# Kernel tuning notes

Measured on AMD Instinct MI355X. Metric: run time of the kernel, lower is better.

The kernel has to match this reference:

```python
import jax, jax.numpy as jnp
import numpy as np

N_NODES = 100000
N_EDGES = 3200000
EMB_DIM = 128


def setup_inputs() -> dict:
    key = jax.random.key(0)
    k_emb, k_w1, k_w2, k_e = jax.random.split(key, 4)
    emb = jax.random.normal(k_emb, (N_NODES, EMB_DIM), dtype=jnp.float32)
    W1 = jax.random.normal(k_w1, (EMB_DIM, 64), dtype=jnp.float32) * (1.0 / np.sqrt(EMB_DIM))
    b1 = jnp.zeros((64,), dtype=jnp.float32)
    W2 = jax.random.normal(k_w2, (64, 32), dtype=jnp.float32) * (1.0 / np.sqrt(64))
    b2 = jnp.zeros((32,), dtype=jnp.float32)
    edge_index = jax.random.randint(k_e, (2, N_EDGES), 0, N_NODES, dtype=jnp.int64)
    return {"embedding": emb, "W1": W1, "b1": b1, "W2": W2, "b2": b2,
            "edge_index": edge_index}


def gcn_conv(x, W, b, src, dst, n):
    # PyG GCNConv defaults: add self-loops, symmetric normalization D^-1/2 (A+I) D^-1/2,
    # linear transform first, then gather-scale-scatter aggregation, then bias.
    xw = x @ W                                                  # [N, out]
    ones = jnp.ones(src.shape, dtype=xw.dtype)
    deg = jax.ops.segment_sum(ones, dst, num_segments=n) + 1.0  # in-degree + self-loop
    dis = jax.lax.rsqrt(deg)                                    # deg >= 1 always
    norm = dis[src] * dis[dst]                                  # [E]
    agg = jax.ops.segment_sum(xw[src] * norm[:, None], dst, num_segments=n)
    agg = agg + (dis * dis)[:, None] * xw                       # self-loop messages
    return agg + b


def reference(embedding, W1, b1, W2, b2, edge_index):
    n = embedding.shape[0]
    src, dst = edge_index[0], edge_index[1]
    # encode
    h = jax.nn.relu(gcn_conv(embedding, W1, b1, src, dst, n))
    z = gcn_conv(h, W2, b2, src, dst, n)                        # [N, 32]
    # decode: per-edge gather-dot-sigmoid
    logits = jnp.sum(z[src] * z[dst], axis=1)                   # [E]
    return jax.nn.sigmoid(logits)
```

## Files before the change

### kernel.cpp

```cpp
#include <hip/hip_runtime.h>
#include <hip/hip_bf16.h>
#include <math.h>

#define NN 100000
#define NE 3200000
#define NPAD 100096
#define NB 196
#define BN 512
#define EPB 8192
#define NBLK 391

typedef __attribute__((ext_vector_type(8))) short short8;
typedef __attribute__((ext_vector_type(4))) float floatx4;
typedef __attribute__((ext_vector_type(4))) unsigned uint4v;

__device__ __forceinline__ unsigned short bf16_of(float x) {
    __hip_bfloat16 h = __float2bfloat16(x);
    return *(unsigned short*)&h;
}
__device__ __forceinline__ unsigned pack2(float a, float b) {
    return (unsigned)bf16_of(a) | ((unsigned)bf16_of(b) << 16);
}
__device__ __forceinline__ float lo_f(unsigned u) { return __uint_as_float(u << 16); }
__device__ __forceinline__ float hi_f(unsigned u) { return __uint_as_float(u & 0xffff0000u); }
__device__ __forceinline__ void acc8(float* a, uint4v r) {
    a[0] += lo_f(r[0]); a[1] += hi_f(r[0]);
    a[2] += lo_f(r[1]); a[3] += hi_f(r[1]);
    a[4] += lo_f(r[2]); a[5] += hi_f(r[2]);
    a[6] += lo_f(r[3]); a[7] += hi_f(r[3]);
}

__global__ __launch_bounds__(256) void hist_kernel(const int* __restrict__ dst,
                                                   int* __restrict__ blkhist) {
    __shared__ int cnt[NB];
    int t = threadIdx.x;
    for (int i = t; i < NB; i += 256) cnt[i] = 0;
    __syncthreads();
    int e0 = blockIdx.x * EPB;
    int e1 = min(e0 + EPB, NE);
    for (int e = e0 + t; e < e1; e += 256) atomicAdd(&cnt[dst[e] >> 9], 1);
    __syncthreads();
    for (int i = t; i < NB; i += 256) blkhist[i * NBLK + blockIdx.x] = cnt[i];
}

__global__ __launch_bounds__(64) void scanA_kernel(int* __restrict__ blkhist,
                                                   int* __restrict__ totals) {
    int j = blockIdx.x, lane = threadIdx.x;
    int base = j * NBLK;
    int carry = 0;
    for (int c = 0; c < NBLK; c += 64) {
        int b = c + lane;
        int v = (b < NBLK) ? blkhist[base + b] : 0;
        int inc = v;
#pragma unroll
        for (int m = 1; m < 64; m <<= 1) {
            int u = __shfl_up(inc, m, 64);
            if (lane >= m) inc += u;
        }
        if (b < NBLK) blkhist[base + b] = carry + inc - v;
        carry += __shfl(inc, 63, 64);
    }
    if (lane == 0) totals[j] = carry;
}

__global__ __launch_bounds__(256) void scanB_kernel(const int* __restrict__ totals,
                                                    int* __restrict__ bucket_base) {
    __shared__ int sm[NB];
    int t = threadIdx.x;
    if (t < NB) sm[t] = totals[t];
    __syncthreads();
    if (t == 0) {
        int r = 0;
        for (int i = 0; i < NB; ++i) { bucket_base[i] = r; r += sm[i]; }
        bucket_base[NB] = r;
    }
}

__global__ __launch_bounds__(256) void scatter_kernel(const int* __restrict__ src,
                                                      const int* __restrict__ dst,
                                                      const int* __restrict__ blkhist,
                                                      const int* __restrict__ bucket_base,
                                                      int* __restrict__ staged) {
    __shared__ int cnt[NB];
    __shared__ int lbase[NB + 1];
    __shared__ int gbase[NB];
    __shared__ int sbuf[EPB];
    __shared__ unsigned char sbkt[EPB];
    int t = threadIdx.x;
    for (int i = t; i < NB; i += 256) cnt[i] = 0;
    __syncthreads();
    int e0 = blockIdx.x * EPB;
    int e1 = min(e0 + EPB, NE);
    int cn = e1 - e0;
    for (int e = e0 + t; e < e1; e += 256) atomicAdd(&cnt[dst[e] >> 9], 1);
    __syncthreads();
    if (t < 64) {
        int v[4]; int s = 0;
#pragma unroll
        for (int k = 0; k < 4; ++k) { int idx = t * 4 + k; v[k] = (idx < NB) ? cnt[idx] : 0; s += v[k]; }
        int inc = s;
#pragma unroll
        for (int m = 1; m < 64; m <<= 1) {
            int u = __shfl_up(inc, m, 64);
            if (t >= m) inc += u;
        }
        int run = inc - s;
#pragma unroll
        for (int k = 0; k < 4; ++k) { int idx = t * 4 + k; if (idx < NB) lbase[idx] = run; run += v[k]; }
        if (t == 63) lbase[NB] = inc;
    }
    __syncthreads();
    for (int i = t; i < NB; i += 256) {
        gbase[i] = bucket_base[i] + blkhist[i * NBLK + blockIdx.x];
        cnt[i] = lbase[i];
    }
    __syncthreads();
    for (int e = e0 + t; e < e1; e += 256) {
        int s = src[e], d = dst[e];
        int bk = d >> 9;
        int r = atomicAdd(&cnt[bk], 1);
        sbuf[r] = (s << 9) | (d & (BN - 1));
        sbkt[r] = (unsigned char)bk;
    }
    __syncthreads();
    for (int i = t; i < cn; i += 256) {
        int bk = sbkt[i];
        staged[gbase[bk] + i - lbase[bk]] = sbuf[i];
    }
}

__global__ __launch_bounds__(256) void fine_kernel(const int* __restrict__ staged,
                                                   const int* __restrict__ bucket_base,
                                                   int* __restrict__ offset,
                                                   float* __restrict__ dis,
                                                   int* __restrict__ csr_src) {
    __shared__ int hist[BN];
    __shared__ int offs[BN];
    __shared__ int cur[BN];
    int t = threadIdx.x, j = blockIdx.x;
    int bb = bucket_base[j], be = bucket_base[j + 1];
    for (int i = t; i < BN; i += 256) hist[i] = 0;
    __syncthreads();
    for (int e = bb + t; e < be; e += 256) atomicAdd(&hist[staged[e] & (BN - 1)], 1);
    __syncthreads();
    if (t < 64) {
        int v[8]; int s = 0;
#pragma unroll
        for (int k = 0; k < 8; ++k) { v[k] = hist[t * 8 + k]; s += v[k]; }
        int inc = s;
#pragma unroll
        for (int m = 1; m < 64; m <<= 1) {
            int u = __shfl_up(inc, m, 64);
            if (t >= m) inc += u;
        }
        int run = inc - s;
#pragma unroll
        for (int k = 0; k < 8; ++k) { offs[t * 8 + k] = run; run += v[k]; }
    }
    __syncthreads();
    for (int l = t; l < BN; l += 256) {
        cur[l] = offs[l];
        int n = j * BN + l;
        if (n < NN) {
            offset[n] = bb + offs[l];
            dis[n] = rsqrtf((float)hist[l] + 1.0f);
        }
    }
    if (j == NB - 1 && t == 0) offset[NN] = NE;
    __syncthreads();
    for (int e = bb + t; e < be; e += 256) {
        int p = staged[e];
        int r = atomicAdd(&cur[p & (BN - 1)], 1);
        csr_src[bb + r] = p >> 9;
    }
}

__global__ __launch_bounds__(256) void mm1_kernel(const float* __restrict__ x,
                                                  const float* __restrict__ W,
                                                  const float* __restrict__ dis,
                                                  unsigned short* __restrict__ y) {
    __shared__ unsigned short Wt[64][136];
    int t = threadIdx.x;
    for (int i = t; i < 128 * 64; i += 256) {
        int k = i >> 6, n = i & 63;
        Wt[n][k] = bf16_of(W[i]);
    }
    __syncthreads();
    int wave = t >> 6, lane = t & 63;
    int quad = lane >> 4, n16 = lane & 15;
    short8 bfr[4][4];
#pragma unroll
    for (int s = 0; s < 4; ++s)
#pragma unroll
        for (int tt = 0; tt < 4; ++tt)
            bfr[s][tt] = *(const short8*)&Wt[tt * 16 + n16][s * 32 + quad * 8];
    int tile0 = (blockIdx.x * 4 + wave) * 4;
#pragma unroll 1
    for (int it = 0; it < 4; ++it) {
        int tile = tile0 + it;
        if (tile >= 6250) break;
        int m0 = tile * 16;
        const float* xp = x + (size_t)(m0 + n16) * 128 + quad * 8;
        floatx4 acc0 = {0,0,0,0}, acc1 = {0,0,0,0}, acc2 = {0,0,0,0}, acc3 = {0,0,0,0};
#pragma unroll
        for (int s = 0; s < 4; ++s) {
            floatx4 lo = __builtin_nontemporal_load((const floatx4*)(xp + s * 32));
            floatx4 hi = __builtin_nontemporal_load((const floatx4*)(xp + s * 32 + 4));
            short8 a;
            a[0] = (short)bf16_of(lo[0]); a[1] = (short)bf16_of(lo[1]);
            a[2] = (short)bf16_of(lo[2]); a[3] = (short)bf16_of(lo[3]);
            a[4] = (short)bf16_of(hi[0]); a[5] = (short)bf16_of(hi[1]);
            a[6] = (short)bf16_of(hi[2]); a[7] = (short)bf16_of(hi[3]);
            acc0 = __builtin_amdgcn_mfma_f32_16x16x32_bf16(a, bfr[s][0], acc0, 0, 0, 0);
            acc1 = __builtin_amdgcn_mfma_f32_16x16x32_bf16(a, bfr[s][1], acc1, 0, 0, 0);
            acc2 = __builtin_amdgcn_mfma_f32_16x16x32_bf16(a, bfr[s][2], acc2, 0, 0, 0);
            acc3 = __builtin_amdgcn_mfma_f32_16x16x32_bf16(a, bfr[s][3], acc3, 0, 0, 0);
        }
#pragma unroll
        for (int r = 0; r < 4; ++r) {
            int ro = m0 + quad * 4 + r;
            float sc = dis[ro];
            unsigned short* yp = y + (size_t)ro * 64 + n16;
            yp[0]  = bf16_of(acc0[r] * sc);
            yp[16] = bf16_of(acc1[r] * sc);
            yp[32] = bf16_of(acc2[r] * sc);
            yp[48] = bf16_of(acc3[r] * sc);
        }
    }
}

__global__ __launch_bounds__(256) void mm2_kernel(const unsigned short* __restrict__ h,
                                                  const float* __restrict__ W,
                                                  const float* __restrict__ dis,
                                                  unsigned short* __restrict__ y) {
    __shared__ unsigned short Wt[32][72];
    int t = threadIdx.x;
    for (int i = t; i < 64 * 32; i += 256) {
        int k = i >> 5, n = i & 31;
        Wt[n][k] = bf16_of(W[i]);
    }
    __syncthreads();
    int wave = t >> 6, lane = t & 63;
    int quad = lane >> 4, n16 = lane & 15;
    short8 bfr[2][2];
#pragma unroll
    for (int s = 0; s < 2; ++s)
#pragma unroll
        for (int tt = 0; tt < 2; ++tt)
            bfr[s][tt] = *(const short8*)&Wt[tt * 16 + n16][s * 32 + quad * 8];
    int tile0 = (blockIdx.x * 4 + wave) * 4;
#pragma unroll 1
    for (int it = 0; it < 4; ++it) {
        int tile = tile0 + it;
        if (tile >= 6250) break;
        int m0 = tile * 16;
        const unsigned short* hp = h + (size_t)(m0 + n16) * 64 + quad * 8;
        floatx4 acc0 = {0,0,0,0}, acc1 = {0,0,0,0};
#pragma unroll
        for (int s = 0; s < 2; ++s) {
            short8 a = *(const short8*)(hp + s * 32);
            acc0 = __builtin_amdgcn_mfma_f32_16x16x32_bf16(a, bfr[s][0], acc0, 0, 0, 0);
            acc1 = __builtin_amdgcn_mfma_f32_16x16x32_bf16(a, bfr[s][1], acc1, 0, 0, 0);
        }
#pragma unroll
        for (int r = 0; r < 4; ++r) {
            int ro = m0 + quad * 4 + r;
            float sc = dis[ro];
            unsigned short* yp = y + (size_t)ro * 32 + n16;
            yp[0]  = bf16_of(acc0[r] * sc);
            yp[16] = bf16_of(acc1[r] * sc);
        }
    }
}

__global__ __launch_bounds__(256) void agg64_kernel(const uint4v* __restrict__ ys4,
                                                    const float* __restrict__ dis,
                                                    const int* __restrict__ offset,
                                                    const int* __restrict__ csr_src,
                                                    const float* __restrict__ b,
                                                    uint4v* __restrict__ h4) {
    int tid = blockIdx.x * 256 + threadIdx.x;
    int nd = tid >> 3, c = tid & 7;
    if (nd >= NN) return;
    int start = offset[nd], end = offset[nd + 1];
    float acc[8] = {0, 0, 0, 0, 0, 0, 0, 0};
    acc8(acc, ys4[(size_t)nd * 8 + c]);
    if (start < end) {
        int last = end - 1;
        int sk[8];
#pragma unroll
        for (int k = 0; k < 8; ++k) sk[k] = csr_src[min(start + k, last)];
        for (int i = start; i < end; i += 8) {
            uint4v r0 = ys4[(size_t)sk[0] * 8 + c];
            uint4v r1 = ys4[(size_t)sk[1] * 8 + c];
            uint4v r2 = ys4[(size_t)sk[2] * 8 + c];
            uint4v r3 = ys4[(size_t)sk[3] * 8 + c];
            uint4v r4 = ys4[(size_t)sk[4] * 8 + c];
            uint4v r5 = ys4[(size_t)sk[5] * 8 + c];
            uint4v r6 = ys4[(size_t)sk[6] * 8 + c];
            uint4v r7 = ys4[(size_t)sk[7] * 8 + c];
            int i2 = i + 8;
            if (i2 < end) {
#pragma unroll
                for (int k = 0; k < 8; ++k) sk[k] = csr_src[min(i2 + k, last)];
            }
            int rem = end - i;
            acc8(acc, r0);
            if (rem > 1) acc8(acc, r1);
            if (rem > 2) acc8(acc, r2);
            if (rem > 3) acc8(acc, r3);
            if (rem > 4) acc8(acc, r4);
            if (rem > 5) acc8(acc, r5);
            if (rem > 6) acc8(acc, r6);
            if (rem > 7) acc8(acc, r7);
        }
    }
    float ds = dis[nd];
    const float4 bv0 = *(const float4*)&b[c * 8];
    const float4 bv1 = *(const float4*)&b[c * 8 + 4];
    uint4v o;
    o[0] = pack2(fmaxf(fmaf(ds, acc[0], bv0.x), 0.f), fmaxf(fmaf(ds, acc[1], bv0.y), 0.f));
    o[1] = pack2(fmaxf(fmaf(ds, acc[2], bv0.z), 0.f), fmaxf(fmaf(ds, acc[3], bv0.w), 0.f));
    o[2] = pack2(fmaxf(fmaf(ds, acc[4], bv1.x), 0.f), fmaxf(fmaf(ds, acc[5], bv1.y), 0.f));
    o[3] = pack2(fmaxf(fmaf(ds, acc[6], bv1.z), 0.f), fmaxf(fmaf(ds, acc[7], bv1.w), 0.f));
    __builtin_nontemporal_store(o, &h4[(size_t)nd * 8 + c]);
}

__global__ __launch_bounds__(256) void agg32_kernel(const uint4v* __restrict__ ys4,
                                                    const float* __restrict__ dis,
                                                    const int* __restrict__ offset,
                                                    const int* __restrict__ csr_src,
                                                    const float* __restrict__ b,
                                                    uint4v* __restrict__ z4) {
    int tid = blockIdx.x * 256 + threadIdx.x;
    int nd = tid >> 2, c = tid & 3;
    if (nd >= NN) return;
    int start = offset[nd], end = offset[nd + 1];
    float acc[8] = {0, 0, 0, 0, 0, 0, 0, 0};
    acc8(acc, ys4[(size_t)nd * 4 + c]);
    if (start < end) {
        int last = end - 1;
        int sk[8];
#pragma unroll
        for (int k = 0; k < 8; ++k) sk[k] = csr_src[min(start + k, last)];
        for (int i = start; i < end; i += 8) {
            uint4v r0 = ys4[(size_t)sk[0] * 4 + c];
            uint4v r1 = ys4[(size_t)sk[1] * 4 + c];
            uint4v r2 = ys4[(size_t)sk[2] * 4 + c];
            uint4v r3 = ys4[(size_t)sk[3] * 4 + c];
            uint4v r4 = ys4[(size_t)sk[4] * 4 + c];
            uint4v r5 = ys4[(size_t)sk[5] * 4 + c];
            uint4v r6 = ys4[(size_t)sk[6] * 4 + c];
            uint4v r7 = ys4[(size_t)sk[7] * 4 + c];
            int i2 = i + 8;
            if (i2 < end) {
#pragma unroll
                for (int k = 0; k < 8; ++k) sk[k] = csr_src[min(i2 + k, last)];
            }
            int rem = end - i;
            acc8(acc, r0);
            if (rem > 1) acc8(acc, r1);
            if (rem > 2) acc8(acc, r2);
            if (rem > 3) acc8(acc, r3);
            if (rem > 4) acc8(acc, r4);
            if (rem > 5) acc8(acc, r5);
            if (rem > 6) acc8(acc, r6);
            if (rem > 7) acc8(acc, r7);
        }
    }
    float ds = dis[nd];
    const float4 bv0 = *(const float4*)&b[c * 8];
    const float4 bv1 = *(const float4*)&b[c * 8 + 4];
    uint4v o;
    o[0] = pack2(fmaf(ds, acc[0], bv0.x), fmaf(ds, acc[1], bv0.y));
    o[1] = pack2(fmaf(ds, acc[2], bv0.z), fmaf(ds, acc[3], bv0.w));
    o[2] = pack2(fmaf(ds, acc[4], bv1.x), fmaf(ds, acc[5], bv1.y));
    o[3] = pack2(fmaf(ds, acc[6], bv1.z), fmaf(ds, acc[7], bv1.w));
    __builtin_nontemporal_store(o, &z4[(size_t)nd * 4 + c]);
}

__global__ __launch_bounds__(256) void decode_kernel(const uint4v* __restrict__ z4,
                                                     const int* __restrict__ src,
                                                     const int* __restrict__ dst,
                                                     float* __restrict__ out) {
    int tid = blockIdx.x * 256 + threadIdx.x;
    int e = tid >> 2, k = tid & 3;
    if (e >= NE) return;
    int s = __builtin_nontemporal_load(&src[e]);
    int d = __builtin_nontemporal_load(&dst[e]);
    uint4v ra = z4[(size_t)s * 4 + k];
    uint4v rb = z4[(size_t)d * 4 + k];
    float acc;
    acc  = lo_f(ra[0]) * lo_f(rb[0]) + hi_f(ra[0]) * hi_f(rb[0]);
    acc += lo_f(ra[1]) * lo_f(rb[1]) + hi_f(ra[1]) * hi_f(rb[1]);
    acc += lo_f(ra[2]) * lo_f(rb[2]) + hi_f(ra[2]) * hi_f(rb[2]);
    acc += lo_f(ra[3]) * lo_f(rb[3]) + hi_f(ra[3]) * hi_f(rb[3]);
#pragma unroll
    for (int m = 2; m >= 1; m >>= 1) acc += __shfl_xor(acc, m, 4);
    if (k == 0) {
        float v = 1.0f / (1.0f + expf(-acc));
        __builtin_nontemporal_store(v, &out[e]);
    }
}

extern "C" void kernel_launch(void* const* d_in, const int* in_sizes, int n_in,
                              void* d_out, int out_size, void* d_ws, size_t ws_size,
                              hipStream_t stream) {
    const float* emb = (const float*)d_in[0];
    const float* W1  = (const float*)d_in[1];
    const float* b1  = (const float*)d_in[2];
    const float* W2  = (const float*)d_in[3];
    const float* b2  = (const float*)d_in[4];
    const int*   ei  = (const int*)d_in[5];
    const int* src = ei;
    const int* dst = ei + NE;
    float* out = (float*)d_out;

    char* w = (char*)d_ws;
    int*   offset      = (int*)w;           w += (size_t)NPAD * 4;
    float* dis         = (float*)w;         w += (size_t)NPAD * 4;
    int*   bucket_base = (int*)w;           w += 1024;
    int*   totals      = (int*)w;           w += 1024;
    int*   blkhist     = (int*)w;           w += 307200;
    int*   csr_src     = (int*)w;           w += (size_t)NE * 4;
    int*   staged      = (int*)w;           w += (size_t)NE * 4;
    unsigned short* ysbuf = (unsigned short*)w; w += (size_t)NN * 64 * 2;
    unsigned short* h  = (unsigned short*)w;
    unsigned short* ys1 = ysbuf;
    unsigned short* ys2 = ysbuf;
    unsigned short* z   = ysbuf + (size_t)NN * 32;

    hist_kernel<<<NBLK, 256, 0, stream>>>(dst, blkhist);
    scanA_kernel<<<NB, 64, 0, stream>>>(blkhist, totals);
    scanB_kernel<<<1, 256, 0, stream>>>(totals, bucket_base);
    scatter_kernel<<<NBLK, 256, 0, stream>>>(src, dst, blkhist, bucket_base, staged);
    fine_kernel<<<NB, 256, 0, stream>>>(staged, bucket_base, offset, dis, csr_src);

    mm1_kernel<<<391, 256, 0, stream>>>(emb, W1, dis, ys1);
    agg64_kernel<<<(NN * 8) / 256, 256, 0, stream>>>((const uint4v*)ys1, dis, offset, csr_src, b1, (uint4v*)h);

    mm2_kernel<<<391, 256, 0, stream>>>(h, W2, dis, ys2);
    agg32_kernel<<<(NN * 4 + 255) / 256, 256, 0, stream>>>((const uint4v*)ys2, dis, offset, csr_src, b2, (uint4v*)z);

    decode_kernel<<<(NE * 4) / 256, 256, 0, stream>>>((const uint4v*)z, src, dst, out);
}
```

Before: 365.2 us.

## Decode edges via CSR by destination, reusing dst embedding and scattering outputs by edge id

The decode kernel now walks the destination-sorted CSR, so each node's z row is loaded once and reused across its incoming edges. Each edge's sigmoid is written to its original edge index, which requires carrying edge ids through the scatter/fine sort; the staged buffer becomes int2 pairs and a csr_eid array is added. The sort now uses 4096 edges per block and twice as many blocks, and z/h stores become normal cached stores. This adds sort traffic and random output writes in exchange for halving the gather reads in decode; the staged buffer also aliases the ys/h workspace region.

Measured after the change: 491.3 us. 1.35x slower.

```diff
diff --git a/kernel.cpp b/kernel.cpp
--- a/kernel.cpp
+++ b/kernel.cpp
@@ -7,8 +7,8 @@
 #define NPAD 100096
 #define NB 196
 #define BN 512
-#define EPB 8192
-#define NBLK 391
+#define EPB 4096
+#define NBLK 782
 
 typedef __attribute__((ext_vector_type(8))) short short8;
 typedef __attribute__((ext_vector_type(4))) float floatx4;
@@ -28,6 +28,12 @@
     a[2] += lo_f(r[1]); a[3] += hi_f(r[1]);
     a[4] += lo_f(r[2]); a[5] += hi_f(r[2]);
     a[6] += lo_f(r[3]); a[7] += hi_f(r[3]);
+}
+__device__ __forceinline__ float dot8(uint4v a, uint4v b) {
+    return lo_f(a[0]) * lo_f(b[0]) + hi_f(a[0]) * hi_f(b[0])
+         + lo_f(a[1]) * lo_f(b[1]) + hi_f(a[1]) * hi_f(b[1])
+         + lo_f(a[2]) * lo_f(b[2]) + hi_f(a[2]) * hi_f(b[2])
+         + lo_f(a[3]) * lo_f(b[3]) + hi_f(a[3]) * hi_f(b[3]);
 }
 
 __global__ __launch_bounds__(256) void hist_kernel(const int* __restrict__ dst,
@@ -80,11 +86,12 @@
                                                       const int* __restrict__ dst,
                                                       const int* __restrict__ blkhist,
                                                       const int* __restrict__ bucket_base,
-                                                      int* __restrict__ staged) {
+                                                      int2* __restrict__ staged) {
     __shared__ int cnt[NB];
     __shared__ int lbase[NB + 1];
     __shared__ int gbase[NB];
-    __shared__ int sbuf[EPB];
+    __shared__ int sbufs[EPB];
+    __shared__ int sbufe[EPB];
     __shared__ unsigned char sbkt[EPB];
     int t = threadIdx.x;
     for (int i = t; i < NB; i += 256) cnt[i] = 0;
@@ -119,21 +126,23 @@
         int s = src[e], d = dst[e];
         int bk = d >> 9;
         int r = atomicAdd(&cnt[bk], 1);
-        sbuf[r] = (s << 9) | (d & (BN - 1));
+        sbufs[r] = (s << 9) | (d & (BN - 1));
+        sbufe[r] = e;
         sbkt[r] = (unsigned char)bk;
     }
     __syncthreads();
     for (int i = t; i < cn; i += 256) {
         int bk = sbkt[i];
-        staged[gbase[bk] + i - lbase[bk]] = sbuf[i];
-    }
-}
-
-__global__ __launch_bounds__(256) void fine_kernel(const int* __restrict__ staged,
+        staged[gbase[bk] + i - lbase[bk]] = make_int2(sbufs[i], sbufe[i]);
+    }
+}
+
+__global__ __launch_bounds__(256) void fine_kernel(const int2* __restrict__ staged,
                                                    const int* __restrict__ bucket_base,
                                                    int* __restrict__ offset,
                                                    float* __restrict__ dis,
-                                                   int* __restrict__ csr_src) {
+                                                   int* __restrict__ csr_src,
+                                                   int* __restrict__ csr_eid) {
     __shared__ int hist[BN];
     __shared__ int offs[BN];
     __shared__ int cur[BN];
@@ -141,7 +150,7 @@
     int bb = bucket_base[j], be = bucket_base[j + 1];
     for (int i = t; i < BN; i += 256) hist[i] = 0;
     __syncthreads();
-    for (int e = bb + t; e < be; e += 256) atomicAdd(&hist[staged[e] & (BN - 1)], 1);
+    for (int e = bb + t; e < be; e += 256) atomicAdd(&hist[staged[e].x & (BN - 1)], 1);
     __syncthreads();
     if (t < 64) {
         int v[8]; int s = 0;
@@ -169,9 +178,10 @@
     if (j == NB - 1 && t == 0) offset[NN] = NE;
     __syncthreads();
     for (int e = bb + t; e < be; e += 256) {
-        int p = staged[e];
-        int r = atomicAdd(&cur[p & (BN - 1)], 1);
-        csr_src[bb + r] = p >> 9;
+        int2 p = staged[e];
+        int r = atomicAdd(&cur[p.x & (BN - 1)], 1);
+        csr_src[bb + r] = p.x >> 9;
+        csr_eid[bb + r] = p.y;
     }
 }
 
@@ -323,7 +333,7 @@
     o[1] = pack2(fmaxf(fmaf(ds, acc[2], bv0.z), 0.f), fmaxf(fmaf(ds, acc[3], bv0.w), 0.f));
     o[2] = pack2(fmaxf(fmaf(ds, acc[4], bv1.x), 0.f), fmaxf(fmaf(ds, acc[5], bv1.y), 0.f));
     o[3] = pack2(fmaxf(fmaf(ds, acc[6], bv1.z), 0.f), fmaxf(fmaf(ds, acc[7], bv1.w), 0.f));
-    __builtin_nontemporal_store(o, &h4[(size_t)nd * 8 + c]);
+    h4[(size_t)nd * 8 + c] = o;
 }
 
 __global__ __launch_bounds__(256) void agg32_kernel(const uint4v* __restrict__ ys4,
@@ -376,30 +386,59 @@
     o[1] = pack2(fmaf(ds, acc[2], bv0.z), fmaf(ds, acc[3], bv0.w));
     o[2] = pack2(fmaf(ds, acc[4], bv1.x), fmaf(ds, acc[5], bv1.y));
     o[3] = pack2(fmaf(ds, acc[6], bv1.z), fmaf(ds, acc[7], bv1.w));
-    __builtin_nontemporal_store(o, &z4[(size_t)nd * 4 + c]);
-}
-
-__global__ __launch_bounds__(256) void decode_kernel(const uint4v* __restrict__ z4,
-                                                     const int* __restrict__ src,
-                                                     const int* __restrict__ dst,
-                                                     float* __restrict__ out) {
+    z4[(size_t)nd * 4 + c] = o;
+}
+
+__global__ __launch_bounds__(256) void decode_csr_kernel(const uint4v* __restrict__ z4,
+                                                         const int* __restrict__ offset,
+                                                         const int* __restrict__ csr_src,
+                                                         const int* __restrict__ csr_eid,
+                                                         float* __restrict__ out) {
     int tid = blockIdx.x * 256 + threadIdx.x;
-    int e = tid >> 2, k = tid & 3;
-    if (e >= NE) return;
-    int s = __builtin_nontemporal_load(&src[e]);
-    int d = __builtin_nontemporal_load(&dst[e]);
-    uint4v ra = z4[(size_t)s * 4 + k];
-    uint4v rb = z4[(size_t)d * 4 + k];
-    float acc;
-    acc  = lo_f(ra[0]) * lo_f(rb[0]) + hi_f(ra[0]) * hi_f(rb[0]);
-    acc += lo_f(ra[1]) * lo_f(rb[1]) + hi_f(ra[1]) * hi_f(rb[1]);
-    acc += lo_f(ra[2]) * lo_f(rb[2]) + hi_f(ra[2]) * hi_f(rb[2]);
-    acc += lo_f(ra[3]) * lo_f(rb[3]) + hi_f(ra[3]) * hi_f(rb[3]);
-#pragma unroll
-    for (int m = 2; m >= 1; m >>= 1) acc += __shfl_xor(acc, m, 4);
-    if (k == 0) {
-        float v = 1.0f / (1.0f + expf(-acc));
-        __builtin_nontemporal_store(v, &out[e]);
+    int nd = tid >> 2, k = tid & 3;
+    if (nd >= NN) return;
+    int start = offset[nd], end = offset[nd + 1];
+    if (start >= end) return;
+    uint4v zd = z4[(size_t)nd * 4 + k];
+    int last = end - 1;
+    int sk[8], ek[8];
+#pragma unroll
+    for (int q = 0; q < 8; ++q) sk[q] = csr_src[min(start + q, last)];
+#pragma unroll
+    for (int q = 0; q < 8; ++q) ek[q] = csr_eid[min(start + q, last)];
+    for (int i = start; i < end; i += 8) {
+        uint4v r0 = z4[(size_t)sk[0] * 4 + k];
+        uint4v r1 = z4[(size_t)sk[1] * 4 + k];
+        uint4v r2 = z4[(size_t)sk[2] * 4 + k];
+        uint4v r3 = z4[(size_t)sk[3] * 4 + k];
+        uint4v r4 = z4[(size_t)sk[4] * 4 + k];
+        uint4v r5 = z4[(size_t)sk[5] * 4 + k];
+        uint4v r6 = z4[(size_t)sk[6] * 4 + k];
+        uint4v r7 = z4[(size_t)sk[7] * 4 + k];
+        int ec0 = ek[0], ec1 = ek[1], ec2 = ek[2], ec3 = ek[3];
+        int ec4 = ek[4], ec5 = ek[5], ec6 = ek[6], ec7 = ek[7];
+        int i2 = i + 8;
+        if (i2 < end) {
+#pragma unroll
+            for (int q = 0; q < 8; ++q) sk[q] = csr_src[min(i2 + q, last)];
+#pragma unroll
+            for (int q = 0; q < 8; ++q) ek[q] = csr_eid[min(i2 + q, last)];
+        }
+        float d0 = dot8(zd, r0), d1 = dot8(zd, r1), d2 = dot8(zd, r2), d3 = dot8(zd, r3);
+        float d4 = dot8(zd, r4), d5 = dot8(zd, r5), d6 = dot8(zd, r6), d7 = dot8(zd, r7);
+#pragma unroll
+        for (int m = 2; m >= 1; m >>= 1) {
+            d0 += __shfl_xor(d0, m, 4); d1 += __shfl_xor(d1, m, 4);
+            d2 += __shfl_xor(d2, m, 4); d3 += __shfl_xor(d3, m, 4);
+            d4 += __shfl_xor(d4, m, 4); d5 += __shfl_xor(d5, m, 4);
+            d6 += __shfl_xor(d6, m, 4); d7 += __shfl_xor(d7, m, 4);
+        }
+        float va = (k & 2) ? ((k & 1) ? d3 : d2) : ((k & 1) ? d1 : d0);
+        float vb = (k & 2) ? ((k & 1) ? d7 : d6) : ((k & 1) ? d5 : d4);
+        int ea = (k & 2) ? ((k & 1) ? ec3 : ec2) : ((k & 1) ? ec1 : ec0);
+        int eb = (k & 2) ? ((k & 1) ? ec7 : ec6) : ((k & 1) ? ec5 : ec4);
+        if (i + k < end)     out[ea] = 1.0f / (1.0f + expf(-va));
+        if (i + 4 + k < end) out[eb] = 1.0f / (1.0f + expf(-vb));
     }
 }
 
@@ -421,11 +460,12 @@
     float* dis         = (float*)w;         w += (size_t)NPAD * 4;
     int*   bucket_base = (int*)w;           w += 1024;
     int*   totals      = (int*)w;           w += 1024;
-    int*   blkhist     = (int*)w;           w += 307200;
+    int*   blkhist     = (int*)w;           w += (size_t)NB * NBLK * 4;
     int*   csr_src     = (int*)w;           w += (size_t)NE * 4;
-    int*   staged      = (int*)w;           w += (size_t)NE * 4;
-    unsigned short* ysbuf = (unsigned short*)w; w += (size_t)NN * 64 * 2;
-    unsigned short* h  = (unsigned short*)w;
+    int*   csr_eid     = (int*)w;           w += (size_t)NE * 4;
+    int2*  staged64    = (int2*)w;
+    unsigned short* ysbuf = (unsigned short*)w;
+    unsigned short* h  = (unsigned short*)(w + (size_t)NE * 4);
     unsigned short* ys1 = ysbuf;
     unsigned short* ys2 = ysbuf;
     unsigned short* z   = ysbuf + (size_t)NN * 32;
@@ -433,8 +473,8 @@
     hist_kernel<<<NBLK, 256, 0, stream>>>(dst, blkhist);
     scanA_kernel<<<NB, 64, 0, stream>>>(blkhist, totals);
     scanB_kernel<<<1, 256, 0, stream>>>(totals, bucket_base);
-    scatter_kernel<<<NBLK, 256, 0, stream>>>(src, dst, blkhist, bucket_base, staged);
-    fine_kernel<<<NB, 256, 0, stream>>>(staged, bucket_base, offset, dis, csr_src);
+    scatter_kernel<<<NBLK, 256, 0, stream>>>(src, dst, blkhist, bucket_base, staged64);
+    fine_kernel<<<NB, 256, 0, stream>>>(staged64, bucket_base, offset, dis, csr_src, csr_eid);
 
     mm1_kernel<<<391, 256, 0, stream>>>(emb, W1, dis, ys1);
     agg64_kernel<<<(NN * 8) / 256, 256, 0, stream>>>((const uint4v*)ys1, dis, offset, csr_src, b1, (uint4v*)h);
@@ -442,5 +482,5 @@
     mm2_kernel<<<391, 256, 0, stream>>>(h, W2, dis, ys2);
     agg32_kernel<<<(NN * 4 + 255) / 256, 256, 0, stream>>>((const uint4v*)ys2, dis, offset, csr_src, b2, (uint4v*)z);
 
-    decode_kernel<<<(NE * 4) / 256, 256, 0, stream>>>((const uint4v*)z, src, dst, out);
-}
+    decode_csr_kernel<<<(NN * 4 + 255) / 256, 256, 0, stream>>>((const uint4v*)z, offset, csr_src, csr_eid, out);
+}
```

## Use finer 128-node buckets for CSR build and drop nontemporal hints

Applied to the files above, without the earlier changes.

Shrinks the CSR-construction buckets from 512 to 128 nodes and halves edges per block. This gives more blocks in the scatter and fine-sort stages and smaller per-bucket work, and the local scan is widened to span all four waves. Separately, the nontemporal loads and stores in mm1, the aggregation kernels and decode become ordinary accesses so the z and h buffers can stay in cache for later kernels. In exchange the block histogram grows, scanB's single-thread serial prefix is four times longer, and scatter needs more shared memory for its wider bucket tags.

Result: slower. 415.0 us (+13.6%).

```diff
diff --git a/kernel.cpp b/kernel.cpp
--- a/kernel.cpp
+++ b/kernel.cpp
@@ -5,10 +5,10 @@
 #define NN 100000
 #define NE 3200000
 #define NPAD 100096
-#define NB 196
-#define BN 512
-#define EPB 8192
-#define NBLK 391
+#define NB 782
+#define BN 128
+#define EPB 4096
+#define NBLK 782
 
 typedef __attribute__((ext_vector_type(8))) short short8;
 typedef __attribute__((ext_vector_type(4))) float floatx4;
@@ -38,7 +38,7 @@
     __syncthreads();
     int e0 = blockIdx.x * EPB;
     int e1 = min(e0 + EPB, NE);
-    for (int e = e0 + t; e < e1; e += 256) atomicAdd(&cnt[dst[e] >> 9], 1);
+    for (int e = e0 + t; e < e1; e += 256) atomicAdd(&cnt[dst[e] >> 7], 1);
     __syncthreads();
     for (int i = t; i < NB; i += 256) blkhist[i * NBLK + blockIdx.x] = cnt[i];
 }
@@ -67,7 +67,7 @@
                                                     int* __restrict__ bucket_base) {
     __shared__ int sm[NB];
     int t = threadIdx.x;
-    if (t < NB) sm[t] = totals[t];
+    for (int i = t; i < NB; i += 256) sm[i] = totals[i];
     __syncthreads();
     if (t == 0) {
         int r = 0;
@@ -85,29 +85,35 @@
     __shared__ int lbase[NB + 1];
     __shared__ int gbase[NB];
     __shared__ int sbuf[EPB];
-    __shared__ unsigned char sbkt[EPB];
+    __shared__ unsigned short sbkt[EPB];
+    __shared__ int wtot[4];
     int t = threadIdx.x;
     for (int i = t; i < NB; i += 256) cnt[i] = 0;
     __syncthreads();
     int e0 = blockIdx.x * EPB;
     int e1 = min(e0 + EPB, NE);
     int cn = e1 - e0;
-    for (int e = e0 + t; e < e1; e += 256) atomicAdd(&cnt[dst[e] >> 9], 1);
-    __syncthreads();
-    if (t < 64) {
+    for (int e = e0 + t; e < e1; e += 256) atomicAdd(&cnt[dst[e] >> 7], 1);
+    __syncthreads();
+    {
         int v[4]; int s = 0;
 #pragma unroll
         for (int k = 0; k < 4; ++k) { int idx = t * 4 + k; v[k] = (idx < NB) ? cnt[idx] : 0; s += v[k]; }
+        int lane = t & 63, wv = t >> 6;
         int inc = s;
 #pragma unroll
         for (int m = 1; m < 64; m <<= 1) {
             int u = __shfl_up(inc, m, 64);
-            if (t >= m) inc += u;
-        }
-        int run = inc - s;
+            if (lane >= m) inc += u;
+        }
+        if (lane == 63) wtot[wv] = inc;
+        __syncthreads();
+        int wbase = 0;
+        for (int w = 0; w < wv; ++w) wbase += wtot[w];
+        int run = wbase + inc - s;
 #pragma unroll
         for (int k = 0; k < 4; ++k) { int idx = t * 4 + k; if (idx < NB) lbase[idx] = run; run += v[k]; }
-        if (t == 63) lbase[NB] = inc;
+        if (t == 255) lbase[NB] = run;
     }
     __syncthreads();
     for (int i = t; i < NB; i += 256) {
@@ -117,10 +123,10 @@
     __syncthreads();
     for (int e = e0 + t; e < e1; e += 256) {
         int s = src[e], d = dst[e];
-        int bk = d >> 9;
+        int bk = d >> 7;
         int r = atomicAdd(&cnt[bk], 1);
-        sbuf[r] = (s << 9) | (d & (BN - 1));
-        sbkt[r] = (unsigned char)bk;
+        sbuf[r] = (s << 7) | (d & (BN - 1));
+        sbkt[r] = (unsigned short)bk;
     }
     __syncthreads();
     for (int i = t; i < cn; i += 256) {
@@ -144,9 +150,9 @@
     for (int e = bb + t; e < be; e += 256) atomicAdd(&hist[staged[e] & (BN - 1)], 1);
     __syncthreads();
     if (t < 64) {
-        int v[8]; int s = 0;
-#pragma unroll
-        for (int k = 0; k < 8; ++k) { v[k] = hist[t * 8 + k]; s += v[k]; }
+        int v[2]; int s = 0;
+#pragma unroll
+        for (int k = 0; k < 2; ++k) { v[k] = hist[t * 2 + k]; s += v[k]; }
         int inc = s;
 #pragma unroll
         for (int m = 1; m < 64; m <<= 1) {
@@ -155,7 +161,7 @@
         }
         int run = inc - s;
 #pragma unroll
-        for (int k = 0; k < 8; ++k) { offs[t * 8 + k] = run; run += v[k]; }
+        for (int k = 0; k < 2; ++k) { offs[t * 2 + k] = run; run += v[k]; }
     }
     __syncthreads();
     for (int l = t; l < BN; l += 256) {
@@ -171,7 +177,7 @@
     for (int e = bb + t; e < be; e += 256) {
         int p = staged[e];
         int r = atomicAdd(&cur[p & (BN - 1)], 1);
-        csr_src[bb + r] = p >> 9;
+        csr_src[bb + r] = p >> 7;
     }
 }
 
@@ -204,13 +210,13 @@
         floatx4 acc0 = {0,0,0,0}, acc1 = {0,0,0,0}, acc2 = {0,0,0,0}, acc3 = {0,0,0,0};
 #pragma unroll
         for (int s = 0; s < 4; ++s) {
-            floatx4 lo = __builtin_nontemporal_load((const floatx4*)(xp + s * 32));
-            floatx4 hi = __builtin_nontemporal_load((const floatx4*)(xp + s * 32 + 4));
+            float4 lo = *(const float4*)(xp + s * 32);
+            float4 hi = *(const float4*)(xp + s * 32 + 4);
             short8 a;
-            a[0] = (short)bf16_of(lo[0]); a[1] = (short)bf16_of(lo[1]);
-            a[2] = (short)bf16_of(lo[2]); a[3] = (short)bf16_of(lo[3]);
-            a[4] = (short)bf16_of(hi[0]); a[5] = (short)bf16_of(hi[1]);
-            a[6] = (short)bf16_of(hi[2]); a[7] = (short)bf16_of(hi[3]);
+            a[0] = (short)bf16_of(lo.x); a[1] = (short)bf16_of(lo.y);
+            a[2] = (short)bf16_of(lo.z); a[3] = (short)bf16_of(lo.w);
+            a[4] = (short)bf16_of(hi.x); a[5] = (short)bf16_of(hi.y);
+            a[6] = (short)bf16_of(hi.z); a[7] = (short)bf16_of(hi.w);
             acc0 = __builtin_amdgcn_mfma_f32_16x16x32_bf16(a, bfr[s][0], acc0, 0, 0, 0);
             acc1 = __builtin_amdgcn_mfma_f32_16x16x32_bf16(a, bfr[s][1], acc1, 0, 0, 0);
             acc2 = __builtin_amdgcn_mfma_f32_16x16x32_bf16(a, bfr[s][2], acc2, 0, 0, 0);
@@ -323,7 +329,7 @@
     o[1] = pack2(fmaxf(fmaf(ds, acc[2], bv0.z), 0.f), fmaxf(fmaf(ds, acc[3], bv0.w), 0.f));
     o[2] = pack2(fmaxf(fmaf(ds, acc[4], bv1.x), 0.f), fmaxf(fmaf(ds, acc[5], bv1.y), 0.f));
     o[3] = pack2(fmaxf(fmaf(ds, acc[6], bv1.z), 0.f), fmaxf(fmaf(ds, acc[7], bv1.w), 0.f));
-    __builtin_nontemporal_store(o, &h4[(size_t)nd * 8 + c]);
+    h4[(size_t)nd * 8 + c] = o;
 }
 
 __global__ __launch_bounds__(256) void agg32_kernel(const uint4v* __restrict__ ys4,
@@ -376,7 +382,7 @@
     o[1] = pack2(fmaf(ds, acc[2], bv0.z), fmaf(ds, acc[3], bv0.w));
     o[2] = pack2(fmaf(ds, acc[4], bv1.x), fmaf(ds, acc[5], bv1.y));
     o[3] = pack2(fmaf(ds, acc[6], bv1.z), fmaf(ds, acc[7], bv1.w));
-    __builtin_nontemporal_store(o, &z4[(size_t)nd * 4 + c]);
+    z4[(size_t)nd * 4 + c] = o;
 }
 
 __global__ __launch_bounds__(256) void decode_kernel(const uint4v* __restrict__ z4,
@@ -386,8 +392,7 @@
     int tid = blockIdx.x * 256 + threadIdx.x;
     int e = tid >> 2, k = tid & 3;
     if (e >= NE) return;
-    int s = __builtin_nontemporal_load(&src[e]);
-    int d = __builtin_nontemporal_load(&dst[e]);
+    int s = src[e], d = dst[e];
     uint4v ra = z4[(size_t)s * 4 + k];
     uint4v rb = z4[(size_t)d * 4 + k];
     float acc;
@@ -397,10 +402,7 @@
     acc += lo_f(ra[3]) * lo_f(rb[3]) + hi_f(ra[3]) * hi_f(rb[3]);
 #pragma unroll
     for (int m = 2; m >= 1; m >>= 1) acc += __shfl_xor(acc, m, 4);
-    if (k == 0) {
-        float v = 1.0f / (1.0f + expf(-acc));
-        __builtin_nontemporal_store(v, &out[e]);
-    }
+    if (k == 0) out[e] = 1.0f / (1.0f + expf(-acc));
 }
 
 extern "C" void kernel_launch(void* const* d_in, const int* in_sizes, int n_in,
@@ -419,9 +421,9 @@
     char* w = (char*)d_ws;
     int*   offset      = (int*)w;           w += (size_t)NPAD * 4;
     float* dis         = (float*)w;         w += (size_t)NPAD * 4;
-    int*   bucket_base = (int*)w;           w += 1024;
-    int*   totals      = (int*)w;           w += 1024;
-    int*   blkhist     = (int*)w;           w += 307200;
+    int*   bucket_base = (int*)w;           w += 4096;
+    int*   totals      = (int*)w;           w += 4096;
+    int*   blkhist     = (int*)w;           w += (size_t)NB * NBLK * 4;
     int*   csr_src     = (int*)w;           w += (size_t)NE * 4;
     int*   staged      = (int*)w;           w += (size_t)NE * 4;
     unsigned short* ysbuf = (unsigned short*)w; w += (size_t)NN * 64 * 2;
```
